# Optimization experiments

Hardware: AMD Instinct MI355X
Metric: run time of the kernel (lower is better)

Reference implementation:

```python
import jax, jax.numpy as jnp
import numpy as np

N = 20000      # nodes
E = 320000     # edges (avg degree 16)
IN = 128
HID = 64
CLS = 32
H0, H1, H2 = 4, 4, 6
SLOPE = 0.2


def _lin(key, fan_in, fan_out):
    kw, kb = jax.random.split(key)
    s = 1.0 / np.sqrt(fan_in)
    W = jax.random.uniform(kw, (fan_in, fan_out), minval=-s, maxval=s, dtype=jnp.float32)
    b = jax.random.uniform(kb, (fan_out,), minval=-s, maxval=s, dtype=jnp.float32)
    return W, b


def setup_inputs() -> dict:
    key = jax.random.key(0)
    ks = jax.random.split(key, 16)
    x = jax.random.normal(ks[0], (N, IN), dtype=jnp.float32)
    src = jax.random.randint(ks[1], (E,), 0, N)
    dst = jax.random.randint(ks[2], (E,), 0, N)
    W0s, b0s = _lin(ks[3], IN, H0 * HID)
    W0d, b0d = _lin(ks[4], IN, H0 * HID)
    a0 = jax.random.normal(ks[5], (H0, HID), dtype=jnp.float32) * 0.05
    d1 = H0 * HID  # 256, flattened hidden width
    W1s, b1s = _lin(ks[6], d1, H1 * HID)
    W1d, b1d = _lin(ks[7], d1, H1 * HID)
    a1 = jax.random.normal(ks[8], (H1, HID), dtype=jnp.float32) * 0.05
    W2s, b2s = _lin(ks[9], d1, H2 * CLS)
    W2d, b2d = _lin(ks[10], d1, H2 * CLS)
    a2 = jax.random.normal(ks[11], (H2, CLS), dtype=jnp.float32) * 0.05
    Wr2, br2 = _lin(ks[12], d1, H2 * CLS)  # residual projection (256 != 192)
    return dict(x=x, src=src, dst=dst,
                W0s=W0s, b0s=b0s, W0d=W0d, b0d=b0d, a0=a0,
                W1s=W1s, b1s=b1s, W1d=W1d, b1d=b1d, a1=a1,
                W2s=W2s, b2s=b2s, W2d=W2d, b2d=b2d, a2=a2,
                Wr2=Wr2, br2=br2)


def _gatv2_layer(x, src, dst, Ws, bs, Wd, bd, attn, heads, dim, res, act):
    n = x.shape[0]
    feat_src = (x @ Ws + bs).reshape(n, heads, dim)
    feat_dst = (x @ Wd + bd).reshape(n, heads, dim)
    # GATv2 edge scores: a^T LeakyReLU(W_l h_u + W_r h_v)
    e = jax.nn.leaky_relu(feat_src[src] + feat_dst[dst], SLOPE)  # [E,H,D]
    logits = jnp.einsum('ehd,hd->eh', e, attn)                    # [E,H]
    # numerically-stable edge softmax over incoming edges per destination
    m = jax.ops.segment_max(logits, dst, num_segments=n)
    m = jnp.where(jnp.isfinite(m), m, 0.0)
    ex = jnp.exp(logits - m[dst])
    denom = jax.ops.segment_sum(ex, dst, num_segments=n)
    alpha = ex / denom[dst]                                        # [E,H]
    out = jax.ops.segment_sum(feat_src[src] * alpha[:, :, None], dst, num_segments=n)
    if res == 'id':
        out = out + x.reshape(n, heads, dim)
    elif res is not None:
        Wr, br = res
        out = out + (x @ Wr + br).reshape(n, heads, dim)
    if act:
        out = jax.nn.elu(out)
    return out  # [n, heads, dim]


def reference(x, src, dst,
              W0s, b0s, W0d, b0d, a0,
              W1s, b1s, W1d, b1d, a1,
              W2s, b2s, W2d, b2d, a2,
              Wr2, br2):
    h = _gatv2_layer(x, src, dst, W0s, b0s, W0d, b0d, a0, H0, HID, None, True)
    h = h.reshape(N, H0 * HID)
    h = _gatv2_layer(h, src, dst, W1s, b1s, W1d, b1d, a1, H1, HID, 'id', True)
    h = h.reshape(N, H1 * HID)
    out = _gatv2_layer(h, src, dst, W2s, b2s, W2d, b2d, a2, H2, CLS, (Wr2, br2), False)
    return out.mean(axis=1)  # [N, num_classes]
```

## Files before the change

kernel.cpp:

```cpp
#include <hip/hip_runtime.h>
#include <hip/hip_bf16.h>
#include <float.h>
#include <math.h>

#define NN 20000
#define EE 320000
#define IN_DIM 128
#define SLOPE_ 0.2f

typedef __attribute__((ext_vector_type(4))) float f32x4;
typedef _Float16 f16;
typedef __attribute__((ext_vector_type(2))) _Float16 f16x2;
typedef __attribute__((ext_vector_type(4))) _Float16 f16x4;
typedef __attribute__((ext_vector_type(8))) _Float16 f16x8;
typedef unsigned short ushort;

__device__ inline void prep_elem(const float* __restrict__ Wa, const float* __restrict__ ba, int na,
                                 const float* __restrict__ Wb, const float* __restrict__ bb, int nb,
                                 const float* __restrict__ Wc, const float* __restrict__ bc, int nc,
                                 int K, f16* __restrict__ Wt, float* __restrict__ bias_cat, int idx) {
    int n = idx / K;
    int k = idx - n * K;
    const float* W; const float* b; int nl; int ncols;
    if (n < na) { W = Wa; b = ba; nl = n; ncols = na; }
    else if (n < na + nb) { W = Wb; b = bb; nl = n - na; ncols = nb; }
    else { W = Wc; b = bc; nl = n - na - nb; ncols = nc; }
    Wt[(size_t)n * K + k] = (f16)W[(size_t)k * ncols + nl];
    if (k == 0) bias_cat[n] = b[nl];
}

#define SEG0 (512 * 128)
#define SEG1 (512 * 256)
#define SEG2 (576 * 256)
#define SEG3 (NN * IN_DIM / 4)
#define SEG4 (NN)
__global__ void prep_all(const float* __restrict__ W0s, const float* __restrict__ b0s,
                         const float* __restrict__ W0d, const float* __restrict__ b0d,
                         const float* __restrict__ W1s, const float* __restrict__ b1s,
                         const float* __restrict__ W1d, const float* __restrict__ b1d,
                         const float* __restrict__ W2s, const float* __restrict__ b2s,
                         const float* __restrict__ W2d, const float* __restrict__ b2d,
                         const float* __restrict__ Wr2, const float* __restrict__ br2,
                         const float* __restrict__ x,
                         f16* __restrict__ Wt0, float* __restrict__ bias0,
                         f16* __restrict__ Wt1, float* __restrict__ bias1,
                         f16* __restrict__ Wt2, float* __restrict__ bias2,
                         f16* __restrict__ A, unsigned int* __restrict__ deg) {
    int idx = blockIdx.x * 256 + threadIdx.x;
    if (idx < SEG0) {
        prep_elem(W0s, b0s, 256, W0d, b0d, 256, nullptr, nullptr, 0, 128, Wt0, bias0, idx);
    } else if ((idx -= SEG0) < SEG1) {
        prep_elem(W1s, b1s, 256, W1d, b1d, 256, nullptr, nullptr, 0, 256, Wt1, bias1, idx);
    } else if ((idx -= SEG1) < SEG2) {
        prep_elem(W2s, b2s, 192, W2d, b2d, 192, Wr2, br2, 192, 256, Wt2, bias2, idx);
    } else if ((idx -= SEG2) < SEG3) {
        float4 v = ((const float4*)x)[idx];
        f16x4 o = {(f16)v.x, (f16)v.y, (f16)v.z, (f16)v.w};
        ((f16x4*)A)[idx] = o;
    } else if ((idx -= SEG3) < SEG4) {
        deg[idx] = 0u;
    }
}

__global__ __launch_bounds__(256) void gemm_mfma_f16(
        const f16* __restrict__ A, const f16* __restrict__ Wt,
        const float* __restrict__ bias,
        f16* __restrict__ F0, f16* __restrict__ F1, float* __restrict__ F2,
        int b1, int b2, int M, int K, int S, int gx, int gy) {
    __shared__ f16 Bs[64 * 256];
    __shared__ f16 Cs[4][32 * 66];

    const int bid = blockIdx.x;
    const int p = bid & 7;
    const int q = bid >> 3;
    const int bn_i = q % gx;
    const int bm_i = (q / gx) * 8 + p;
    if (bm_i >= gy) return;
    const int bm = bm_i * 256;
    const int bn = bn_i * 64;

    const int tid = threadIdx.x;
    const int wave = tid >> 6;
    const int lane = tid & 63;
    const int m16 = lane & 15;
    const int quad = lane >> 4;

    {
        const int n = tid >> 2;
        const int q0 = tid & 3;
        for (int j = 0; j * 32 < K; ++j) {
            int k0 = j * 32 + q0 * 8;
            f16x8 v = *(const f16x8*)(Wt + (size_t)(bn + n) * K + k0);
            int chunk = (j * 4 + (n >> 4)) * 64 + q0 * 16 + (n & 15);
            *(f16x8*)&Bs[chunk * 8] = v;
        }
    }
    __syncthreads();

    #pragma unroll
    for (int miter = 0; miter < 2; ++miter) {
        const int rbase = bm + wave * 64 + miter * 32;
        f32x4 acc[2][4];
        #pragma unroll
        for (int i = 0; i < 2; ++i)
            #pragma unroll
            for (int j = 0; j < 4; ++j) acc[i][j] = (f32x4){0.f, 0.f, 0.f, 0.f};

        int ar[2];
        #pragma unroll
        for (int mt = 0; mt < 2; ++mt) {
            int row = rbase + mt * 16 + m16;
            ar[mt] = row < M ? row : M - 1;
        }

        #pragma unroll 4
        for (int k0 = 0; k0 < K; k0 += 32) {
            f16x8 ah[2];
            #pragma unroll
            for (int mt = 0; mt < 2; ++mt)
                ah[mt] = *(const f16x8*)(A + (size_t)ar[mt] * K + k0 + quad * 8);
            #pragma unroll
            for (int nt = 0; nt < 4; ++nt) {
                f16x8 bs = *(const f16x8*)&Bs[(((k0 >> 5) * 4 + nt) * 64 + lane) * 8];
                #pragma unroll
                for (int mt = 0; mt < 2; ++mt)
                    acc[mt][nt] = __builtin_amdgcn_mfma_f32_16x16x32_f16(ah[mt], bs, acc[mt][nt], 0, 0, 0);
            }
        }

        if (bn < b2) {
            f16* __restrict__ Fb;
            int cs, cb;
            if (bn >= b1) { Fb = F1; cb = bn - b1; cs = b2 - b1; }
            else          { Fb = F0; cb = bn;      cs = b1; }
            f16* cw = &Cs[wave][0];
            #pragma unroll
            for (int nt = 0; nt < 4; ++nt) {
                float bv = bias[bn + nt * 16 + m16];
                #pragma unroll
                for (int mt = 0; mt < 2; ++mt)
                    #pragma unroll
                    for (int r = 0; r < 4; ++r) {
                        int row = mt * 16 + quad * 4 + r;
                        cw[row * 66 + nt * 16 + m16] = (f16)(acc[mt][nt][r] + bv);
                    }
            }
            int lrow = lane >> 1;
            int lcol = (lane & 1) * 32;
            int grow = rbase + lrow;
            if (grow < M) {
                #pragma unroll
                for (int j = 0; j < 4; ++j) {
                    f16x8 v = *(f16x8*)&cw[lrow * 66 + lcol + j * 8];
                    *(f16x8*)&Fb[(size_t)grow * cs + cb + lcol + j * 8] = v;
                }
            }
        } else {
            int cs = S - b2;
            #pragma unroll
            for (int nt = 0; nt < 4; ++nt) {
                int col = bn - b2 + nt * 16 + m16;
                float bv = bias[bn + nt * 16 + m16];
                #pragma unroll
                for (int mt = 0; mt < 2; ++mt)
                    #pragma unroll
                    for (int r = 0; r < 4; ++r) {
                        int row = rbase + mt * 16 + quad * 4 + r;
                        if (row < M) F2[(size_t)row * cs + col] = acc[mt][nt][r] + bv;
                    }
            }
        }
    }
}

__global__ void hist_dst(const int* __restrict__ dst, unsigned int* __restrict__ deg, int E) {
    int e = blockIdx.x * blockDim.x + threadIdx.x;
    if (e < E) atomicAdd(&deg[dst[e]], 1u);
}

__global__ __launch_bounds__(1024) void scan_fast(const unsigned int* __restrict__ deg,
                                                  unsigned int* __restrict__ row_ptr,
                                                  unsigned int* __restrict__ cursor, int n) {
    __shared__ unsigned int vals[NN];
    __shared__ unsigned int sums[1024];
    const int t = threadIdx.x;
    for (int i = t; i < n; i += 1024) vals[i] = deg[i];
    __syncthreads();
    const int chunk = (n + 1023) / 1024;
    const int start = t * chunk;
    const int end = min(start + chunk, n);
    unsigned int s = 0;
    for (int i = start; i < end; ++i) { unsigned int d = vals[i]; vals[i] = s; s += d; }
    sums[t] = s;
    __syncthreads();
    for (int off = 1; off < 1024; off <<= 1) {
        unsigned int v = (t >= off) ? sums[t - off] : 0u;
        __syncthreads();
        sums[t] += v;
        __syncthreads();
    }
    const unsigned int prefix = (t == 0) ? 0u : sums[t - 1];
    for (int i = start; i < end; ++i) vals[i] += prefix;
    __syncthreads();
    for (int i = t; i < n; i += 1024) {
        unsigned int v = vals[i];
        row_ptr[i] = v;
        cursor[i] = v;
    }
    if (t == 1023) row_ptr[n] = sums[1023];
}

__global__ void scatter_edges(const int* __restrict__ src, const int* __restrict__ dst,
                              unsigned int* __restrict__ cursor,
                              int* __restrict__ csr_src, int E) {
    int e = blockIdx.x * blockDim.x + threadIdx.x;
    if (e < E) {
        unsigned int pos = atomicAdd(&cursor[dst[e]], 1u);
        csr_src[pos] = src[e];
    }
}

template <int HD, int D, bool HAS_RES, bool DO_ELU, int OUT_MODE>
__global__ __launch_bounds__(256) void gat_node_aggregate(
        const f16* __restrict__ fsb, const f16* __restrict__ fdb,
        const float* __restrict__ attn,
        const unsigned int* __restrict__ row_ptr,
        const int* __restrict__ csr_src,
        const float* __restrict__ resid, int RS,
        float* __restrict__ outF, f16* __restrict__ outA) {
    constexpr int LANES = HD / 8;
    constexpr int GSZ = D / 8;
    __shared__ float red[(OUT_MODE == 2) ? 8 : 1][(OUT_MODE == 2) ? HD : 1];

    const int wave = threadIdx.x >> 6;
    const int lane = threadIdx.x & 63;
    const int half = lane >> 5;
    const int ln = lane & 31;
    const int t = blockIdx.x * 8 + wave * 2 + half;
    const bool active = (ln < LANES);
    const unsigned off = active ? 8u * ln : 0u;

    f16x2 fdp[4], a6p[4], a4p[4];
    if (active) {
        f16x8 dv = *(const f16x8*)&fdb[(unsigned)t * HD + off];
        float4 aA = *(const float4*)&attn[off];
        float4 aB = *(const float4*)&attn[off + 4];
        float av[8] = {aA.x, aA.y, aA.z, aA.w, aB.x, aB.y, aB.z, aB.w};
        #pragma unroll
        for (int i = 0; i < 4; ++i) {
            fdp[i] = (f16x2){dv[2 * i], dv[2 * i + 1]};
            a6p[i] = (f16x2){(f16)(0.6f * av[2 * i]), (f16)(0.6f * av[2 * i + 1])};
            a4p[i] = (f16x2){(f16)(0.4f * av[2 * i]), (f16)(0.4f * av[2 * i + 1])};
        }
    } else {
        #pragma unroll
        for (int i = 0; i < 4; ++i) {
            fdp[i] = (f16x2){0, 0};
            a6p[i] = (f16x2){0, 0};
            a4p[i] = (f16x2){0, 0};
        }
    }

    const int jj0 = (int)row_ptr[t];
    const int jj1 = (int)row_ptr[t + 1];
    const int deg = jj1 - jj0;
    const int last = jj1 - 1;
    const int degO = __shfl_xor(deg, 32, 64);
    const int mdeg = max(deg, degO);

    float acc[8];
    #pragma unroll
    for (int d = 0; d < 8; ++d) acc[d] = 0.f;
    float lh = 0.f;

    f16x8 buf[8];
    int cidx[8];
    #pragma unroll
    for (int u = 0; u < 8; ++u) {
        int e0 = min(jj0 + u, last);
        buf[u] = *(const f16x8*)&fsb[(unsigned)csr_src[e0] * HD + off];
        cidx[u] = csr_src[min(jj0 + 8 + u, last)];
    }

    for (int b = 0; b < mdeg; b += 8) {
        #pragma unroll
        for (int u = 0; u < 8; ++u) {
            const f16x8 cur = buf[u];
            buf[u] = *(const f16x8*)&fsb[(unsigned)cidx[u] * HD + off];
            cidx[u] = csr_src[min(jj0 + b + 16 + u, last)];
            float p = 0.f;
            #pragma unroll
            for (int i = 0; i < 4; ++i) {
                f16x2 cp = (f16x2){cur[2 * i], cur[2 * i + 1]};
                f16x2 xp = cp + fdp[i];
                unsigned xu = __builtin_bit_cast(unsigned, xp) & 0x7FFF7FFFu;
                f16x2 xa = __builtin_bit_cast(f16x2, xu);
                p = __builtin_amdgcn_fdot2(xp, a6p[i], p, false);
                p = __builtin_amdgcn_fdot2(xa, a4p[i], p, false);
            }
            #pragma unroll
            for (int o = 1; o < GSZ; o <<= 1)
                p += __shfl_xor(p, o, 64);
            float w = (b + u < deg) ? __expf(p) : 0.f;
            lh += w;
            #pragma unroll
            for (int d = 0; d < 8; ++d) acc[d] += w * (float)cur[d];
        }
    }

    float inv = (lh > 0.f) ? 1.f / lh : 0.f;
    float vout[8];
    #pragma unroll
    for (int d = 0; d < 8; ++d) vout[d] = acc[d] * inv;
    if (HAS_RES && active) {
        float4 rA = *(const float4*)&resid[(unsigned)t * RS + off];
        float4 rB = *(const float4*)&resid[(unsigned)t * RS + off + 4];
        vout[0] += rA.x; vout[1] += rA.y; vout[2] += rA.z; vout[3] += rA.w;
        vout[4] += rB.x; vout[5] += rB.y; vout[6] += rB.z; vout[7] += rB.w;
    }
    if (DO_ELU) {
        #pragma unroll
        for (int d = 0; d < 8; ++d) vout[d] = vout[d] > 0.f ? vout[d] : expm1f(vout[d]);
    }

    if (OUT_MODE == 2) {
        const int nib = wave * 2 + half;
        if (active) {
            *(float4*)&red[nib][off] = make_float4(vout[0], vout[1], vout[2], vout[3]);
            *(float4*)&red[nib][off + 4] = make_float4(vout[4], vout[5], vout[6], vout[7]);
        }
        __syncthreads();
        int node = threadIdx.x >> 5;
        int col = threadIdx.x & 31;
        float ssum = 0.f;
        #pragma unroll
        for (int h = 0; h < 6; ++h) ssum += red[node][h * 32 + col];
        outF[(unsigned)(blockIdx.x * 8 + node) * 32 + col] = ssum * (1.f / 6.f);
    } else if (active) {
        f16x8 av;
        #pragma unroll
        for (int d = 0; d < 8; ++d) av[d] = (f16)vout[d];
        *(f16x8*)&outA[(unsigned)t * HD + off] = av;
        if (OUT_MODE == 0) {
            *(float4*)&outF[(unsigned)t * HD + off] = make_float4(vout[0], vout[1], vout[2], vout[3]);
            *(float4*)&outF[(unsigned)t * HD + off + 4] = make_float4(vout[4], vout[5], vout[6], vout[7]);
        }
    }
}

extern "C" void kernel_launch(void* const* d_in, const int* in_sizes, int n_in,
                              void* d_out, int out_size, void* d_ws, size_t ws_size,
                              hipStream_t stream) {
    const float* x   = (const float*)d_in[0];
    const int*   src = (const int*)d_in[1];
    const int*   dst = (const int*)d_in[2];
    const float* W0s = (const float*)d_in[3];
    const float* b0s = (const float*)d_in[4];
    const float* W0d = (const float*)d_in[5];
    const float* b0d = (const float*)d_in[6];
    const float* a0  = (const float*)d_in[7];
    const float* W1s = (const float*)d_in[8];
    const float* b1s = (const float*)d_in[9];
    const float* W1d = (const float*)d_in[10];
    const float* b1d = (const float*)d_in[11];
    const float* a1  = (const float*)d_in[12];
    const float* W2s = (const float*)d_in[13];
    const float* b2s = (const float*)d_in[14];
    const float* W2d = (const float*)d_in[15];
    const float* b2d = (const float*)d_in[16];
    const float* a2  = (const float*)d_in[17];
    const float* Wr2 = (const float*)d_in[18];
    const float* br2 = (const float*)d_in[19];

    f16* FsH = (f16*)d_ws;
    f16* FdH = FsH + (size_t)NN * 256;
    f16* A   = FdH + (size_t)NN * 256;
    float* O0 = (float*)(A + (size_t)NN * 256);
    f16* Wt0 = (f16*)(O0 + (size_t)NN * 256);
    f16* Wt1 = Wt0 + 512 * 128;
    f16* Wt2 = Wt1 + 512 * 256;
    float* bias0 = (float*)(Wt2 + 576 * 256);
    float* bias1 = bias0 + 512;
    float* bias2 = bias1 + 512;
    unsigned int* row_ptr = (unsigned int*)(bias2 + 576);
    unsigned int* cursor  = row_ptr + (NN + 1);
    unsigned int* deg     = cursor + NN;
    int* csr_src          = (int*)(deg + NN);

    {
        int total = SEG0 + SEG1 + SEG2 + SEG3 + SEG4;
        prep_all<<<(total + 255) / 256, 256, 0, stream>>>(
            W0s, b0s, W0d, b0d, W1s, b1s, W1d, b1d, W2s, b2s, W2d, b2d, Wr2, br2, x,
            Wt0, bias0, Wt1, bias1, Wt2, bias2, A, deg);
    }
    hist_dst<<<(EE + 255) / 256, 256, 0, stream>>>(dst, deg, EE);
    scan_fast<<<1, 1024, 0, stream>>>(deg, row_ptr, cursor, NN);
    scatter_edges<<<(EE + 255) / 256, 256, 0, stream>>>(src, dst, cursor, csr_src, EE);

    const int gy = (NN + 255) / 256;
    const int gy8 = ((gy + 7) / 8) * 8;
    const int nagg = NN / 8;

    gemm_mfma_f16<<<gy8 * 8, 256, 0, stream>>>(A, Wt0, bias0,
                                               FsH, FdH, nullptr, 256, 512, NN, 128, 512, 8, gy);
    gat_node_aggregate<256, 64, false, true, 0><<<nagg, 256, 0, stream>>>(
        FsH, FdH, a0, row_ptr, csr_src, nullptr, 0, O0, A);

    gemm_mfma_f16<<<gy8 * 8, 256, 0, stream>>>(A, Wt1, bias1,
                                               FsH, FdH, nullptr, 256, 512, NN, 256, 512, 8, gy);
    gat_node_aggregate<256, 64, true, true, 1><<<nagg, 256, 0, stream>>>(
        FsH, FdH, a1, row_ptr, csr_src, O0, 256, nullptr, A);

    gemm_mfma_f16<<<gy8 * 9, 256, 0, stream>>>(A, Wt2, bias2,
                                               FsH, FdH, O0, 192, 384, NN, 256, 576, 9, gy);
    gat_node_aggregate<192, 32, true, false, 2><<<nagg, 256, 0, stream>>>(
        FsH, FdH, a2, row_ptr, csr_src, O0, 192, (float*)d_out, nullptr);
}
```

Measured before the change: 307.8 us.

## Fuse histogram and edge scatter into existing kernels, restructure GEMM and aggregation loops

Moves the destination-degree histogram into the prep kernel, with the degree reset done by a memset, and runs the CSR edge scatter as extra blocks appended to the first GEMM launch. This removes two kernel launches. The GEMM now computes both 32-row sub-tiles in one k-loop, so each B fragment loaded from LDS is reused across more MFMAs, at the cost of more accumulator registers. The aggregation edge loop handles its second group of 4 edges only when it exists, which skips padded work for low-degree nodes but adds a branch.

```diff
diff --git a/kernel.cpp b/kernel.cpp
--- a/kernel.cpp
+++ b/kernel.cpp
@@ -33,7 +33,7 @@
 #define SEG1 (512 * 256)
 #define SEG2 (576 * 256)
 #define SEG3 (NN * IN_DIM / 4)
-#define SEG4 (NN)
+#define SEG4 (EE)
 __global__ void prep_all(const float* __restrict__ W0s, const float* __restrict__ b0s,
                          const float* __restrict__ W0d, const float* __restrict__ b0d,
                          const float* __restrict__ W1s, const float* __restrict__ b1s,
@@ -41,7 +41,7 @@
                          const float* __restrict__ W2s, const float* __restrict__ b2s,
                          const float* __restrict__ W2d, const float* __restrict__ b2d,
                          const float* __restrict__ Wr2, const float* __restrict__ br2,
-                         const float* __restrict__ x,
+                         const float* __restrict__ x, const int* __restrict__ dst,
                          f16* __restrict__ Wt0, float* __restrict__ bias0,
                          f16* __restrict__ Wt1, float* __restrict__ bias1,
                          f16* __restrict__ Wt2, float* __restrict__ bias2,
@@ -58,7 +58,7 @@
         f16x4 o = {(f16)v.x, (f16)v.y, (f16)v.z, (f16)v.w};
         ((f16x4*)A)[idx] = o;
     } else if ((idx -= SEG3) < SEG4) {
-        deg[idx] = 0u;
+        atomicAdd(&deg[dst[idx]], 1u);
     }
 }
 
@@ -66,11 +66,22 @@
         const f16* __restrict__ A, const f16* __restrict__ Wt,
         const float* __restrict__ bias,
         f16* __restrict__ F0, f16* __restrict__ F1, float* __restrict__ F2,
-        int b1, int b2, int M, int K, int S, int gx, int gy) {
+        int b1, int b2, int M, int K, int S, int gx, int gy,
+        int GB, const int* __restrict__ esrc, const int* __restrict__ edst,
+        unsigned int* __restrict__ cursor, int* __restrict__ csr_src, int E) {
     __shared__ f16 Bs[64 * 256];
     __shared__ f16 Cs[4][32 * 66];
 
     const int bid = blockIdx.x;
+    if (bid >= GB) {
+        int e = (bid - GB) * 256 + threadIdx.x;
+        if (e < E) {
+            unsigned int pos = atomicAdd(&cursor[edst[e]], 1u);
+            csr_src[pos] = esrc[e];
+        }
+        return;
+    }
+
     const int p = bid & 7;
     const int q = bid >> 3;
     const int bn_i = q % gx;
@@ -97,37 +108,47 @@
     }
     __syncthreads();
 
-    #pragma unroll
-    for (int miter = 0; miter < 2; ++miter) {
-        const int rbase = bm + wave * 64 + miter * 32;
-        f32x4 acc[2][4];
-        #pragma unroll
-        for (int i = 0; i < 2; ++i)
+    const int rb0 = bm + wave * 64;
+    f32x4 acc[2][2][4];
+    #pragma unroll
+    for (int mi = 0; mi < 2; ++mi)
+        #pragma unroll
+        for (int mt = 0; mt < 2; ++mt)
             #pragma unroll
-            for (int j = 0; j < 4; ++j) acc[i][j] = (f32x4){0.f, 0.f, 0.f, 0.f};
-
-        int ar[2];
+            for (int nt = 0; nt < 4; ++nt) acc[mi][mt][nt] = (f32x4){0.f, 0.f, 0.f, 0.f};
+
+    int ar[2][2];
+    #pragma unroll
+    for (int mi = 0; mi < 2; ++mi)
         #pragma unroll
         for (int mt = 0; mt < 2; ++mt) {
-            int row = rbase + mt * 16 + m16;
-            ar[mt] = row < M ? row : M - 1;
-        }
-
-        #pragma unroll 4
-        for (int k0 = 0; k0 < K; k0 += 32) {
+            int row = rb0 + mi * 32 + mt * 16 + m16;
+            ar[mi][mt] = row < M ? row : M - 1;
+        }
+
+    #pragma unroll 2
+    for (int k0 = 0; k0 < K; k0 += 32) {
+        f16x8 bs[4];
+        #pragma unroll
+        for (int nt = 0; nt < 4; ++nt)
+            bs[nt] = *(const f16x8*)&Bs[(((k0 >> 5) * 4 + nt) * 64 + lane) * 8];
+        #pragma unroll
+        for (int mi = 0; mi < 2; ++mi) {
             f16x8 ah[2];
             #pragma unroll
             for (int mt = 0; mt < 2; ++mt)
-                ah[mt] = *(const f16x8*)(A + (size_t)ar[mt] * K + k0 + quad * 8);
+                ah[mt] = *(const f16x8*)(A + (size_t)ar[mi][mt] * K + k0 + quad * 8);
             #pragma unroll
-            for (int nt = 0; nt < 4; ++nt) {
-                f16x8 bs = *(const f16x8*)&Bs[(((k0 >> 5) * 4 + nt) * 64 + lane) * 8];
+            for (int nt = 0; nt < 4; ++nt)
                 #pragma unroll
                 for (int mt = 0; mt < 2; ++mt)
-                    acc[mt][nt] = __builtin_amdgcn_mfma_f32_16x16x32_f16(ah[mt], bs, acc[mt][nt], 0, 0, 0);
-            }
-        }
-
+                    acc[mi][mt][nt] = __builtin_amdgcn_mfma_f32_16x16x32_f16(ah[mt], bs[nt], acc[mi][mt][nt], 0, 0, 0);
+        }
+    }
+
+    #pragma unroll
+    for (int mi = 0; mi < 2; ++mi) {
+        const int rbase = rb0 + mi * 32;
         if (bn < b2) {
             f16* __restrict__ Fb;
             int cs, cb;
@@ -142,7 +163,7 @@
                     #pragma unroll
                     for (int r = 0; r < 4; ++r) {
                         int row = mt * 16 + quad * 4 + r;
-                        cw[row * 66 + nt * 16 + m16] = (f16)(acc[mt][nt][r] + bv);
+                        cw[row * 66 + nt * 16 + m16] = (f16)(acc[mi][mt][nt][r] + bv);
                     }
             }
             int lrow = lane >> 1;
@@ -166,16 +187,11 @@
                     #pragma unroll
                     for (int r = 0; r < 4; ++r) {
                         int row = rbase + mt * 16 + quad * 4 + r;
-                        if (row < M) F2[(size_t)row * cs + col] = acc[mt][nt][r] + bv;
+                        if (row < M) F2[(size_t)row * cs + col] = acc[mi][mt][nt][r] + bv;
                     }
             }
         }
     }
-}
-
-__global__ void hist_dst(const int* __restrict__ dst, unsigned int* __restrict__ deg, int E) {
-    int e = blockIdx.x * blockDim.x + threadIdx.x;
-    if (e < E) atomicAdd(&deg[dst[e]], 1u);
 }
 
 __global__ __launch_bounds__(1024) void scan_fast(const unsigned int* __restrict__ deg,
@@ -210,15 +226,30 @@
     if (t == 1023) row_ptr[n] = sums[1023];
 }
 
-__global__ void scatter_edges(const int* __restrict__ src, const int* __restrict__ dst,
-                              unsigned int* __restrict__ cursor,
-                              int* __restrict__ csr_src, int E) {
-    int e = blockIdx.x * blockDim.x + threadIdx.x;
-    if (e < E) {
-        unsigned int pos = atomicAdd(&cursor[dst[e]], 1u);
-        csr_src[pos] = src[e];
-    }
-}
+#define AGG_STEP4(U0)                                                         \
+    _Pragma("unroll")                                                         \
+    for (int uu = 0; uu < 4; ++uu) {                                          \
+        const int u = (U0) + uu;                                              \
+        const f16x8 cur = buf[u];                                             \
+        buf[u] = *(const f16x8*)&fsb[(unsigned)cidx[u] * HD + off];           \
+        cidx[u] = csr_src[min(jj0 + b + 16 + u, last)];                       \
+        float p = 0.f;                                                        \
+        _Pragma("unroll")                                                     \
+        for (int i = 0; i < 4; ++i) {                                         \
+            f16x2 cp = (f16x2){cur[2 * i], cur[2 * i + 1]};                   \
+            f16x2 xp = cp + fdp[i];                                           \
+            unsigned xu = __builtin_bit_cast(unsigned, xp) & 0x7FFF7FFFu;     \
+            f16x2 xa = __builtin_bit_cast(f16x2, xu);                         \
+            p = __builtin_amdgcn_fdot2(xp, a6p[i], p, false);                 \
+            p = __builtin_amdgcn_fdot2(xa, a4p[i], p, false);                 \
+        }                                                                     \
+        _Pragma("unroll")                                                     \
+        for (int o = 1; o < GSZ; o <<= 1) p += __shfl_xor(p, o, 64);          \
+        float w = (b + u < deg) ? __expf(p) : 0.f;                            \
+        lh += w;                                                              \
+        _Pragma("unroll")                                                     \
+        for (int d = 0; d < 8; ++d) acc[d] += w * (float)cur[d];              \
+    }
 
 template <int HD, int D, bool HAS_RES, bool DO_ELU, int OUT_MODE>
 __global__ __launch_bounds__(256) void gat_node_aggregate(
@@ -283,28 +314,9 @@
     }
 
     for (int b = 0; b < mdeg; b += 8) {
-        #pragma unroll
-        for (int u = 0; u < 8; ++u) {
-            const f16x8 cur = buf[u];
-            buf[u] = *(const f16x8*)&fsb[(unsigned)cidx[u] * HD + off];
-            cidx[u] = csr_src[min(jj0 + b + 16 + u, last)];
-            float p = 0.f;
-            #pragma unroll
-            for (int i = 0; i < 4; ++i) {
-                f16x2 cp = (f16x2){cur[2 * i], cur[2 * i + 1]};
-                f16x2 xp = cp + fdp[i];
-                unsigned xu = __builtin_bit_cast(unsigned, xp) & 0x7FFF7FFFu;
-                f16x2 xa = __builtin_bit_cast(f16x2, xu);
-                p = __builtin_amdgcn_fdot2(xp, a6p[i], p, false);
-                p = __builtin_amdgcn_fdot2(xa, a4p[i], p, false);
-            }
-            #pragma unroll
-            for (int o = 1; o < GSZ; o <<= 1)
-                p += __shfl_xor(p, o, 64);
-            float w = (b + u < deg) ? __expf(p) : 0.f;
-            lh += w;
-            #pragma unroll
-            for (int d = 0; d < 8; ++d) acc[d] += w * (float)cur[d];
+        AGG_STEP4(0)
+        if (b + 4 < mdeg) {
+            AGG_STEP4(4)
         }
     }
 
@@ -387,32 +399,35 @@
     unsigned int* deg     = cursor + NN;
     int* csr_src          = (int*)(deg + NN);
 
+    hipMemsetAsync(deg, 0, NN * sizeof(unsigned int), stream);
     {
         int total = SEG0 + SEG1 + SEG2 + SEG3 + SEG4;
         prep_all<<<(total + 255) / 256, 256, 0, stream>>>(
-            W0s, b0s, W0d, b0d, W1s, b1s, W1d, b1d, W2s, b2s, W2d, b2d, Wr2, br2, x,
+            W0s, b0s, W0d, b0d, W1s, b1s, W1d, b1d, W2s, b2s, W2d, b2d, Wr2, br2, x, dst,
             Wt0, bias0, Wt1, bias1, Wt2, bias2, A, deg);
     }
-    hist_dst<<<(EE + 255) / 256, 256, 0, stream>>>(dst, deg, EE);
     scan_fast<<<1, 1024, 0, stream>>>(deg, row_ptr, cursor, NN);
-    scatter_edges<<<(EE + 255) / 256, 256, 0, stream>>>(src, dst, cursor, csr_src, EE);
 
     const int gy = (NN + 255) / 256;
     const int gy8 = ((gy + 7) / 8) * 8;
     const int nagg = NN / 8;
-
-    gemm_mfma_f16<<<gy8 * 8, 256, 0, stream>>>(A, Wt0, bias0,
-                                               FsH, FdH, nullptr, 256, 512, NN, 128, 512, 8, gy);
+    const int sblk = (EE + 255) / 256;
+
+    gemm_mfma_f16<<<gy8 * 8 + sblk, 256, 0, stream>>>(A, Wt0, bias0,
+                                               FsH, FdH, nullptr, 256, 512, NN, 128, 512, 8, gy,
+                                               gy8 * 8, src, dst, cursor, csr_src, EE);
     gat_node_aggregate<256, 64, false, true, 0><<<nagg, 256, 0, stream>>>(
         FsH, FdH, a0, row_ptr, csr_src, nullptr, 0, O0, A);
 
     gemm_mfma_f16<<<gy8 * 8, 256, 0, stream>>>(A, Wt1, bias1,
-                                               FsH, FdH, nullptr, 256, 512, NN, 256, 512, 8, gy);
+                                               FsH, FdH, nullptr, 256, 512, NN, 256, 512, 8, gy,
+                                               gy8 * 8, nullptr, nullptr, nullptr, nullptr, 0);
     gat_node_aggregate<256, 64, true, true, 1><<<nagg, 256, 0, stream>>>(
         FsH, FdH, a1, row_ptr, csr_src, O0, 256, nullptr, A);
 
     gemm_mfma_f16<<<gy8 * 9, 256, 0, stream>>>(A, Wt2, bias2,
-                                               FsH, FdH, O0, 192, 384, NN, 256, 576, 9, gy);
+                                               FsH, FdH, O0, 192, 384, NN, 256, 576, 9, gy,
+                                               gy8 * 9, nullptr, nullptr, nullptr, nullptr, 0);
     gat_node_aggregate<192, 32, true, false, 2><<<nagg, 256, 0, stream>>>(
         FsH, FdH, a2, row_ptr, csr_src, O0, 192, (float*)d_out, nullptr);
 }
```

Measured after the change: 300.4 us. 1.02x faster.
